# Kernel tuning notes

Hardware: AMD Instinct MI355X
Metric: run time of the kernel (lower is better)

## Reference

```python
import jax, jax.numpy as jnp
import numpy as np

B, N_PER, P_PER = 64, 64, 2016   # graphs, nodes/graph, pairs/graph (C(64,2))
IN_DIM, HID, OUT = 64, 128, 10
EDGE_P = 0.125


def _build_graph_structures():
    """Integer preprocessing replicating build_2sets_from_embeddings's
    combinatorics (pairs, iso_type source, triangle-based 2-set edges)."""
    rng = np.random.default_rng(0)
    n, b = N_PER, B
    A = rng.random((b, n, n)) < EDGE_P
    A = np.triu(A, 1)
    A = A | A.transpose(0, 2, 1)                      # symmetric, no self loops
    gs, us, vs = np.nonzero(A)                        # directed edges, both dirs
    edge_index = np.stack([gs * n + us, gs * n + vs]).astype(np.int64)
    batch = np.repeat(np.arange(b), n).astype(np.int64)
    iu, iv = np.triu_indices(n, 1)                    # local pair (u<v) lists
    pidx = np.full((n, n), -1, np.int64)
    pidx[iu, iv] = np.arange(P_PER)
    pidx[iv, iu] = np.arange(P_PER)                   # symmetric lookup = sorted()
    pair_u = (np.arange(b)[:, None] * n + iu[None, :]).ravel().astype(np.int64)
    pair_v = (np.arange(b)[:, None] * n + iv[None, :]).ravel().astype(np.int64)
    iso_type = A[:, iu, iv].astype(np.float32).ravel()[:, None]  # [B*P_PER,1]
    # 2-set edges: pair (u,v) -> sorted(v,w) and sorted(u,w) for every common
    # neighbor w of u and v (matches _build_2set_edges exactly)
    common = A[:, iu, :] & A[:, iv, :]                # (B, P_PER, n)
    g2, ps, ws = np.nonzero(common)
    u, v = iu[ps], iv[ps]
    d1 = pidx[v, ws]
    d2 = pidx[u, ws]
    src = np.concatenate([g2 * P_PER + ps, g2 * P_PER + ps])
    dst = np.concatenate([g2 * P_PER + d1, g2 * P_PER + d2])
    two_edges = np.stack([src, dst]).astype(np.int64)
    two_batch = np.repeat(np.arange(b), P_PER).astype(np.int64)
    return edge_index, batch, pair_u, pair_v, iso_type, two_edges, two_batch


def setup_inputs() -> dict:
    ei, batch, pu, pv, iso, te, tb = _build_graph_structures()
    key = jax.random.key(0)
    ks = jax.random.split(key, 16)
    w = lambda k, i, o: jax.random.normal(k, (i, o), jnp.float32) / np.float32(np.sqrt(i))
    two_in = 2 * HID + 1
    return {
        "x": jax.random.normal(ks[0], (B * N_PER, IN_DIM), jnp.float32),
        "g1_W1_0": w(ks[1], IN_DIM, HID), "g1_W2_0": w(ks[2], IN_DIM, HID),
        "g1_W1_1": w(ks[3], HID, HID),    "g1_W2_1": w(ks[4], HID, HID),
        "g1_W1_2": w(ks[5], HID, HID),    "g1_W2_2": w(ks[6], HID, HID),
        "k_W1_0": w(ks[7], two_in, HID),  "k_W2_0": w(ks[8], two_in, HID),
        "k_W1_1": w(ks[9], HID, HID),     "k_W2_1": w(ks[10], HID, HID),
        "c_W0": w(ks[11], 2 * HID, HID),  "c_b0": jnp.zeros((HID,), jnp.float32),
        "c_W1": w(ks[12], HID, OUT),      "c_b1": jnp.zeros((OUT,), jnp.float32),
        "iso_type": jnp.asarray(iso),
        "edge_index": jnp.asarray(ei), "batch": jnp.asarray(batch),
        "pair_u": jnp.asarray(pu), "pair_v": jnp.asarray(pv),
        "two_edges": jnp.asarray(te), "two_batch": jnp.asarray(tb),
    }


def _mp_layer(h, ei, W1, W2):
    # relu( h @ W1 + scatter_add_{dst}( h[src] @ W2 ) )  -- OneGNNLayer / KSetLayer
    msg = h[ei[0]] @ W2
    agg = jax.ops.segment_sum(msg, ei[1], num_segments=h.shape[0])
    return jax.nn.relu(h @ W1 + agg)


def reference(x, g1_W1_0, g1_W2_0, g1_W1_1, g1_W2_1, g1_W1_2, g1_W2_2,
              k_W1_0, k_W2_0, k_W1_1, k_W2_1,
              c_W0, c_b0, c_W1, c_b1,
              iso_type, edge_index, batch, pair_u, pair_v, two_edges, two_batch):
    h = _mp_layer(x, edge_index, g1_W1_0, g1_W2_0)
    h = _mp_layer(h, edge_index, g1_W1_1, g1_W2_1)
    h = _mp_layer(h, edge_index, g1_W1_2, g1_W2_2)
    graph_emb_1 = jax.ops.segment_sum(h, batch, num_segments=B)
    # 2-set features: [h_u, h_v, iso_type]  -> [P, 2H+1]
    two_x = jnp.concatenate([h[pair_u], h[pair_v], iso_type], axis=1)
    h2 = _mp_layer(two_x, two_edges, k_W1_0, k_W2_0)
    h2 = _mp_layer(h2, two_edges, k_W1_1, k_W2_1)
    graph_emb_2 = jax.ops.segment_sum(h2, two_batch, num_segments=B)
    combined = jnp.concatenate([graph_emb_1, graph_emb_2], axis=1)
    hc = jax.nn.relu(combined @ c_W0 + c_b0)   # Dropout(p=0.5) inactive in eval
    return hc @ c_W1 + c_b1
```

## Files before the change

kernel.cpp:

```cpp
#include <hip/hip_runtime.h>
#include <hip/hip_bf16.h>


typedef short s16x8 __attribute__((ext_vector_type(8)));
typedef float f32x4 __attribute__((ext_vector_type(4)));

__device__ __forceinline__ unsigned short f2bf(float f) {
  union { float f; unsigned u; } x; x.f = f;
  unsigned r = (x.u + 0x7fffu + ((x.u >> 16) & 1u)) >> 16;
  return (unsigned short)r;
}
__device__ __forceinline__ float bf2f(unsigned short h) {
  union { unsigned u; float f; } x; x.u = ((unsigned)h) << 16;
  return x.f;
}
__device__ __forceinline__ float4 ldbf4(const unsigned short* p) {
  ushort4 q = *(const ushort4*)p;
  return make_float4(bf2f(q.x), bf2f(q.y), bf2f(q.z), bf2f(q.w));
}
__device__ __forceinline__ void stbf4(unsigned short* p, float4 v) {
  ushort4 q;
  q.x = f2bf(v.x); q.y = f2bf(v.y); q.z = f2bf(v.z); q.w = f2bf(v.w);
  *(ushort4*)p = q;
}
__device__ __forceinline__ float4 ld4(const float* p) { return *(const float4*)p; }

template<int KCS, int ASTR>
__device__ __forceinline__ void mfma_dual_lds(
    const unsigned short* A, const unsigned short* Wfrag,
    f32x4 (&accA)[8], f32x4 (&accB)[8])
{
  const int lane = threadIdx.x & 63;
  const int wv = threadIdx.x >> 6;
  const int row = wv * 16 + (lane & 15);
  const int k0 = (lane >> 4) << 3;
  const unsigned short* ap = A + row * ASTR + k0;
  const unsigned short* wp = Wfrag + (size_t)lane * 8;
#pragma unroll
  for (int i = 0; i < 8; ++i) { accA[i] = (f32x4)0.f; accB[i] = (f32x4)0.f; }
#pragma unroll
  for (int kc = 0; kc < KCS; ++kc) {
    s16x8 af = *(const s16x8*)(ap + kc * 32);
#pragma unroll
    for (int nt = 0; nt < 8; ++nt) {
      s16x8 b0 = *(const s16x8*)(wp + ((size_t)((nt)*KCS + kc) << 9));
      s16x8 b1 = *(const s16x8*)(wp + ((size_t)((8 + nt) * KCS + kc) << 9));
      accA[nt] = __builtin_amdgcn_mfma_f32_16x16x32_bf16(af, b0, accA[nt], 0, 0, 0);
      accB[nt] = __builtin_amdgcn_mfma_f32_16x16x32_bf16(af, b1, accB[nt], 0, 0, 0);
    }
  }
}

__device__ __forceinline__ void epi_lds(const f32x4 (&accA)[8], const f32x4 (&accB)[8],
    unsigned short (*preS)[136], unsigned short (*msgS)[136])
{
  const int lane = threadIdx.x & 63;
  const int wv = threadIdx.x >> 6;
  const int col = lane & 15;
  const int r0 = wv * 16 + ((lane >> 4) << 2);
  __syncthreads();
#pragma unroll
  for (int nt = 0; nt < 8; ++nt)
#pragma unroll
    for (int r = 0; r < 4; ++r) {
      preS[r0 + r][nt * 16 + col] = f2bf(accA[nt][r]);
      msgS[r0 + r][nt * 16 + col] = f2bf(accB[nt][r]);
    }
  __syncthreads();
}

__device__ __forceinline__ void epi_global(const f32x4 (&accA)[8], const f32x4 (&accB)[8],
    unsigned short (*sOut)[136], unsigned short* Ca, unsigned short* Cb, long tile)
{
  const int tid = threadIdx.x;
  const int lane = tid & 63;
  const int wv = tid >> 6;
  const int col = lane & 15;
  const int r0 = wv * 16 + ((lane >> 4) << 2);
  const long rowBase = tile * 64;
#pragma unroll
  for (int sel = 0; sel < 2; ++sel) {
    __syncthreads();
#pragma unroll
    for (int nt = 0; nt < 8; ++nt) {
#pragma unroll
      for (int r = 0; r < 4; ++r)
        sOut[r0 + r][nt * 16 + col] = f2bf(sel ? accB[nt][r] : accA[nt][r]);
    }
    __syncthreads();
    unsigned short* C = sel ? Cb : Ca;
#pragma unroll
    for (int i = 0; i < 4; ++i) {
      int fi = tid + i * 256;
      int row = fi >> 4;
      int c8 = fi & 15;
      *(uint4*)(C + (rowBase + row) * 128 + c8 * 8) = *(uint4*)&sOut[row][c8 * 8];
    }
  }
}

struct NArgs {
  const float* x;
  const int* ei;
  const int* gstart;
  const unsigned short *Wf0, *Wf1, *Wf2, *Wf3, *Wf4;
  unsigned short *HU1, *HV1, *HU2, *HV2;
  float* ge1;
  int E1;
};

__global__ __launch_bounds__(256) void node_stage(NArgs a)
{
  __shared__ __align__(16) unsigned short hS[64][136];
  __shared__ __align__(16) unsigned short preS[64][136];
  __shared__ __align__(16) unsigned short msgS[64][136];
  __shared__ int ldeg[64], lcur[64], loff[65];
  __shared__ unsigned short ledge[1024];
  __shared__ float sge[128];

  const int b = blockIdx.x;
  const int t = threadIdx.x;
  const int base = b * 64;

  const int es = a.gstart[b], ee = a.gstart[b + 1];
  if (t < 64) ldeg[t] = 0;
  if (t < 128) sge[t] = 0.f;
  __syncthreads();
  for (int i = es + t; i < ee; i += 256)
    atomicAdd(&ldeg[a.ei[a.E1 + i] - base], 1);
  __syncthreads();
  if (t < 64) {
    int v = ldeg[t], s = v;
#pragma unroll
    for (int d = 1; d < 64; d <<= 1) {
      int o = __shfl_up(s, d, 64);
      if (t >= d) s += o;
    }
    loff[t] = s - v;
    lcur[t] = s - v;
    if (t == 63) loff[64] = s;
  }
  unsigned short* xs = &preS[0][0];
  for (int i = t; i < 64 * 64; i += 256) {
    int r = i >> 6, c = i & 63;
    xs[r * 72 + c] = f2bf(a.x[(size_t)(base + r) * 64 + c]);
  }
  __syncthreads();
  for (int i = es + t; i < ee; i += 256) {
    int s = a.ei[i] - base, d = a.ei[a.E1 + i] - base;
    int pos = atomicAdd(&lcur[d], 1);
    ledge[pos] = (unsigned short)s;
  }
  __syncthreads();

  f32x4 accA[8], accB[8];
  const int grp = t >> 5, f = (t & 31) * 4;

  mfma_dual_lds<2, 72>(xs, a.Wf0, accA, accB);
  epi_lds(accA, accB, preS, msgS);
  for (int r = grp; r < 64; r += 8) {
    float4 acc = ldbf4(&preS[r][f]);
    int j1 = loff[r + 1];
    for (int j = loff[r]; j < j1; ++j) {
      float4 m = ldbf4(&msgS[ledge[j]][f]);
      acc.x += m.x; acc.y += m.y; acc.z += m.z; acc.w += m.w;
    }
    stbf4(&hS[r][f], make_float4(fmaxf(acc.x, 0.f), fmaxf(acc.y, 0.f),
                                 fmaxf(acc.z, 0.f), fmaxf(acc.w, 0.f)));
  }
  __syncthreads();

  mfma_dual_lds<4, 136>(&hS[0][0], a.Wf1, accA, accB);
  epi_lds(accA, accB, preS, msgS);
  for (int r = grp; r < 64; r += 8) {
    float4 acc = ldbf4(&preS[r][f]);
    int j1 = loff[r + 1];
    for (int j = loff[r]; j < j1; ++j) {
      float4 m = ldbf4(&msgS[ledge[j]][f]);
      acc.x += m.x; acc.y += m.y; acc.z += m.z; acc.w += m.w;
    }
    stbf4(&hS[r][f], make_float4(fmaxf(acc.x, 0.f), fmaxf(acc.y, 0.f),
                                 fmaxf(acc.z, 0.f), fmaxf(acc.w, 0.f)));
  }
  __syncthreads();

  mfma_dual_lds<4, 136>(&hS[0][0], a.Wf2, accA, accB);
  epi_lds(accA, accB, preS, msgS);
  {
    float4 g = make_float4(0.f, 0.f, 0.f, 0.f);
    for (int r = grp; r < 64; r += 8) {
      float4 acc = ldbf4(&preS[r][f]);
      int j1 = loff[r + 1];
      for (int j = loff[r]; j < j1; ++j) {
        float4 m = ldbf4(&msgS[ledge[j]][f]);
        acc.x += m.x; acc.y += m.y; acc.z += m.z; acc.w += m.w;
      }
      float4 o = make_float4(fmaxf(acc.x, 0.f), fmaxf(acc.y, 0.f),
                             fmaxf(acc.z, 0.f), fmaxf(acc.w, 0.f));
      stbf4(&hS[r][f], o);
      g.x += o.x; g.y += o.y; g.z += o.z; g.w += o.w;
    }
    atomicAdd(&sge[f + 0], g.x);
    atomicAdd(&sge[f + 1], g.y);
    atomicAdd(&sge[f + 2], g.z);
    atomicAdd(&sge[f + 3], g.w);
  }
  __syncthreads();
  if (t < 128) a.ge1[b * 128 + t] = sge[t];

  mfma_dual_lds<4, 136>(&hS[0][0], a.Wf3, accA, accB);
  epi_global(accA, accB, preS, a.HU1, a.HU2, b);
  mfma_dual_lds<4, 136>(&hS[0][0], a.Wf4, accA, accB);
  epi_global(accA, accB, preS, a.HV1, a.HV2, b);
}

struct PrepArgs {
  const float* wa[6];
  const float* wb[6];
  unsigned short* Wf[6];
  float* ge2;
  const int* te; int E2;
  int* degP;
  const int* ei; int E1;
  int* gstart;
  int nCnt;
};

__global__ void prep(PrepArgs p)
{
  int bb = blockIdx.x, t = threadIdx.x;
  if (bb < 88) {
    int gid = bb * 256 + t;
    if (gid < 22528) {
      int pi, local, kcs, kclog;
      if (gid < 2048) { pi = 0; local = gid; kcs = 2; kclog = 1; }
      else { int r = gid - 2048; pi = 1 + (r >> 12); local = r & 4095; kcs = 4; kclog = 2; }
      int lane = local & 63;
      int t1 = local >> 6;
      int kc = t1 & (kcs - 1);
      int t2 = t1 >> kclog;
      int nt = t2 & 7;
      int wsel = t2 >> 3;
      const float* W = wsel ? p.wb[pi] : p.wa[pi];
      int k0 = kc * 32 + ((lane >> 4) << 3);
      int n = nt * 16 + (lane & 15);
      unsigned short tmp[8];
#pragma unroll
      for (int j = 0; j < 8; ++j) tmp[j] = f2bf(W[(size_t)(k0 + j) * 128 + n]);
      *(uint4*)(p.Wf[pi] + (size_t)local * 8) = *(uint4*)tmp;
    }
  } else if (bb < 120) {
    int i = (bb - 88) * 256 + t;
    if (i < 8192) p.ge2[i] = 0.f;
  } else if (bb < 120 + p.nCnt) {
    int e = (bb - 120) * 256 + t;
    if (e < p.E2) atomicAdd(&p.degP[p.te[p.E2 + e]], 1);
  } else {
    int e = (bb - 120 - p.nCnt) * 256 + t;
    if (e <= p.E1) {
      int ge = (e < p.E1) ? (p.ei[e] >> 6) : 64;
      int gp = (e > 0) ? (p.ei[e - 1] >> 6) : -1;
      for (int g = gp + 1; g <= ge; ++g) p.gstart[g] = e;
    }
  }
}

__global__ __launch_bounds__(256) void scan_reduce(const int* __restrict__ deg,
                                                   int* __restrict__ bsum, int n)
{
  __shared__ int s[256];
  int b = blockIdx.x, t = threadIdx.x;
  int base = b * 1024;
  int v = 0;
#pragma unroll
  for (int i = 0; i < 4; ++i) {
    int idx = base + t + i * 256;
    if (idx < n) v += deg[idx];
  }
  s[t] = v;
  __syncthreads();
  for (int d = 128; d > 0; d >>= 1) {
    if (t < d) s[t] += s[t + d];
    __syncthreads();
  }
  if (t == 0) bsum[b] = s[0];
}

__global__ __launch_bounds__(1024) void scan_partials(int* __restrict__ bsum, int nb)
{
  __shared__ int s[1024];
  int t = threadIdx.x;
  s[t] = (t < nb) ? bsum[t] : 0;
  __syncthreads();
  for (int d = 1; d < 1024; d <<= 1) {
    int v = (t >= d) ? s[t - d] : 0;
    __syncthreads();
    s[t] += v;
    __syncthreads();
  }
  if (t < nb) bsum[t] = (t == 0) ? 0 : s[t - 1];
  if (t == 1023) bsum[nb] = s[1023];
}

__global__ __launch_bounds__(256) void scan_final(const int* __restrict__ deg,
                                                  const int* __restrict__ bsum,
                                                  int* __restrict__ off,
                                                  int* __restrict__ cur, int n, int nb)
{
  __shared__ int s[256];
  int b = blockIdx.x, t = threadIdx.x;
  int base = b * 1024 + t * 4;
  int v0 = 0, v1 = 0, v2 = 0, v3 = 0;
  if (base + 0 < n) v0 = deg[base + 0];
  if (base + 1 < n) v1 = deg[base + 1];
  if (base + 2 < n) v2 = deg[base + 2];
  if (base + 3 < n) v3 = deg[base + 3];
  s[t] = v0 + v1 + v2 + v3;
  __syncthreads();
  for (int d = 1; d < 256; d <<= 1) {
    int v = (t >= d) ? s[t - d] : 0;
    __syncthreads();
    s[t] += v;
    __syncthreads();
  }
  int run = bsum[b] + ((t == 0) ? 0 : s[t - 1]);
  if (base + 0 < n) { off[base + 0] = run; cur[base + 0] = run; run += v0; }
  if (base + 1 < n) { off[base + 1] = run; cur[base + 1] = run; run += v1; }
  if (base + 2 < n) { off[base + 2] = run; cur[base + 2] = run; run += v2; }
  if (base + 3 < n) { off[base + 3] = run; cur[base + 3] = run; run += v3; }
  if (b == 0 && t == 0) off[n] = bsum[nb];
}

__global__ void csr_fill_pair(const int* __restrict__ te, int E2,
                              const int* __restrict__ pu, const int* __restrict__ pv,
                              const float* __restrict__ iso,
                              int* __restrict__ curP, int4* __restrict__ recP)
{
  int e = blockIdx.x * 256 + threadIdx.x;
  if (e >= E2) return;
  int s = te[e], d = te[E2 + e];
  int pos = atomicAdd(&curP[d], 1);
  recP[pos] = make_int4(pu[s], pv[s], __float_as_int(iso[s]), s);
}

struct TGArgs {
  const unsigned short *HU1, *HV1, *HU2, *HV2;
  const float *iso, *w1iso, *w2iso;
  const int *pu, *pv, *off;
  const int4* rec;
  const unsigned short* Wf5;
  unsigned short *PRE2, *MSG2;
};

__global__ __launch_bounds__(256) void two0_gemm(TGArgs a)
{
  __shared__ __align__(16) unsigned short hS[64][136];
  __shared__ int sOff[65];
  __shared__ int sPu[64], sPv[64];
  __shared__ float sIso[64];
  const int t = threadIdx.x;
  const long tile = blockIdx.x;
  const int grp = t >> 5, f = (t & 31) * 4;
  const int pbase = (int)(tile * 64);

  if (t < 65) sOff[t] = a.off[pbase + t];
  if (t >= 64 && t < 128)  sPu[t - 64]  = a.pu[pbase + t - 64];
  if (t >= 128 && t < 192) sPv[t - 128] = a.pv[pbase + t - 128];
  if (t >= 192)            sIso[t - 192] = a.iso[pbase + t - 192];
  __syncthreads();

  float4 wi1 = ld4(a.w1iso + f);
  float4 wi2 = ld4(a.w2iso + f);

#pragma unroll
  for (int pass = 0; pass < 4; ++pass) {
    int rA = grp * 8 + pass * 2;
    int rB = rA + 1;
    float isA = sIso[rA], isB = sIso[rB];
    float4 a1 = ldbf4(a.HU1 + (size_t)sPu[rA] * 128 + f);
    float4 b1 = ldbf4(a.HV1 + (size_t)sPv[rA] * 128 + f);
    float4 a2 = ldbf4(a.HU1 + (size_t)sPu[rB] * 128 + f);
    float4 b2 = ldbf4(a.HV1 + (size_t)sPv[rB] * 128 + f);
    float4 accA, accB;
    accA.x = a1.x + b1.x + isA * wi1.x;
    accA.y = a1.y + b1.y + isA * wi1.y;
    accA.z = a1.z + b1.z + isA * wi1.z;
    accA.w = a1.w + b1.w + isA * wi1.w;
    accB.x = a2.x + b2.x + isB * wi1.x;
    accB.y = a2.y + b2.y + isB * wi1.y;
    accB.z = a2.z + b2.z + isB * wi1.z;
    accB.w = a2.w + b2.w + isB * wi1.w;
    int jA = sOff[rA], eA = sOff[rA + 1];
    int jB = sOff[rB], eB = sOff[rB + 1];
    while (jA < eA && jB < eB) {
      int4 qA = a.rec[jA++];
      int4 qB = a.rec[jB++];
      float4 muA = ldbf4(a.HU2 + (size_t)qA.x * 128 + f);
      float4 mvA = ldbf4(a.HV2 + (size_t)qA.y * 128 + f);
      float4 muB = ldbf4(a.HU2 + (size_t)qB.x * 128 + f);
      float4 mvB = ldbf4(a.HV2 + (size_t)qB.y * 128 + f);
      float iA = __int_as_float(qA.z), iB = __int_as_float(qB.z);
      accA.x += muA.x + mvA.x + iA * wi2.x;
      accA.y += muA.y + mvA.y + iA * wi2.y;
      accA.z += muA.z + mvA.z + iA * wi2.z;
      accA.w += muA.w + mvA.w + iA * wi2.w;
      accB.x += muB.x + mvB.x + iB * wi2.x;
      accB.y += muB.y + mvB.y + iB * wi2.y;
      accB.z += muB.z + mvB.z + iB * wi2.z;
      accB.w += muB.w + mvB.w + iB * wi2.w;
    }
    for (; jA + 1 < eA; jA += 2) {
      int4 q0 = a.rec[jA], q1 = a.rec[jA + 1];
      float4 mu0 = ldbf4(a.HU2 + (size_t)q0.x * 128 + f);
      float4 mv0 = ldbf4(a.HV2 + (size_t)q0.y * 128 + f);
      float4 mu1 = ldbf4(a.HU2 + (size_t)q1.x * 128 + f);
      float4 mv1 = ldbf4(a.HV2 + (size_t)q1.y * 128 + f);
      float i0 = __int_as_float(q0.z), i1 = __int_as_float(q1.z);
      accA.x += mu0.x + mv0.x + i0 * wi2.x + mu1.x + mv1.x + i1 * wi2.x;
      accA.y += mu0.y + mv0.y + i0 * wi2.y + mu1.y + mv1.y + i1 * wi2.y;
      accA.z += mu0.z + mv0.z + i0 * wi2.z + mu1.z + mv1.z + i1 * wi2.z;
      accA.w += mu0.w + mv0.w + i0 * wi2.w + mu1.w + mv1.w + i1 * wi2.w;
    }
    if (jA < eA) {
      int4 q0 = a.rec[jA];
      float4 mu0 = ldbf4(a.HU2 + (size_t)q0.x * 128 + f);
      float4 mv0 = ldbf4(a.HV2 + (size_t)q0.y * 128 + f);
      float i0 = __int_as_float(q0.z);
      accA.x += mu0.x + mv0.x + i0 * wi2.x;
      accA.y += mu0.y + mv0.y + i0 * wi2.y;
      accA.z += mu0.z + mv0.z + i0 * wi2.z;
      accA.w += mu0.w + mv0.w + i0 * wi2.w;
    }
    for (; jB + 1 < eB; jB += 2) {
      int4 q0 = a.rec[jB], q1 = a.rec[jB + 1];
      float4 mu0 = ldbf4(a.HU2 + (size_t)q0.x * 128 + f);
      float4 mv0 = ldbf4(a.HV2 + (size_t)q0.y * 128 + f);
      float4 mu1 = ldbf4(a.HU2 + (size_t)q1.x * 128 + f);
      float4 mv1 = ldbf4(a.HV2 + (size_t)q1.y * 128 + f);
      float i0 = __int_as_float(q0.z), i1 = __int_as_float(q1.z);
      accB.x += mu0.x + mv0.x + i0 * wi2.x + mu1.x + mv1.x + i1 * wi2.x;
      accB.y += mu0.y + mv0.y + i0 * wi2.y + mu1.y + mv1.y + i1 * wi2.y;
      accB.z += mu0.z + mv0.z + i0 * wi2.z + mu1.z + mv1.z + i1 * wi2.z;
      accB.w += mu0.w + mv0.w + i0 * wi2.w + mu1.w + mv1.w + i1 * wi2.w;
    }
    if (jB < eB) {
      int4 q0 = a.rec[jB];
      float4 mu0 = ldbf4(a.HU2 + (size_t)q0.x * 128 + f);
      float4 mv0 = ldbf4(a.HV2 + (size_t)q0.y * 128 + f);
      float i0 = __int_as_float(q0.z);
      accB.x += mu0.x + mv0.x + i0 * wi2.x;
      accB.y += mu0.y + mv0.y + i0 * wi2.y;
      accB.z += mu0.z + mv0.z + i0 * wi2.z;
      accB.w += mu0.w + mv0.w + i0 * wi2.w;
    }
    stbf4(&hS[rA][f], make_float4(fmaxf(accA.x, 0.f), fmaxf(accA.y, 0.f),
                                  fmaxf(accA.z, 0.f), fmaxf(accA.w, 0.f)));
    stbf4(&hS[rB][f], make_float4(fmaxf(accB.x, 0.f), fmaxf(accB.y, 0.f),
                                  fmaxf(accB.z, 0.f), fmaxf(accB.w, 0.f)));
  }
  __syncthreads();

  f32x4 accA[8], accB[8];
  mfma_dual_lds<4, 136>(&hS[0][0], a.Wf5, accA, accB);
  epi_global(accA, accB, hS, a.PRE2, a.MSG2, tile);
}

__global__ __launch_bounds__(256) void gather_segsum(
    const unsigned short* __restrict__ pre, const unsigned short* __restrict__ msg,
    const int* __restrict__ off, const int4* __restrict__ rec,
    float* __restrict__ ge2, int ppg)
{
  __shared__ float sF[128];
  __shared__ int sOff[127];
  int t = threadIdx.x;
  int c = blockIdx.x & 7;
  int k = blockIdx.x >> 3;
  int g = c + 8 * (k & 7);
  int sub = k >> 3;
  int r0 = g * ppg + sub * 126;
  if (t < 128) sF[t] = 0.f;
  if (t < 127) sOff[t] = off[r0 + t];
  __syncthreads();
  int grp = t >> 5, f = (t & 31) * 4;
  const int lim = 126;
  int rbeg = grp * 16;
  int rend = rbeg + 16; if (rend > lim) rend = lim;
  float4 gacc = make_float4(0.f, 0.f, 0.f, 0.f);
  for (int rr = rbeg; rr < rend; rr += 2) {
    int rA = rr, rB = rr + 1;
    bool vB = (rB < rend);
    float4 accA = ldbf4(pre + (size_t)(r0 + rA) * 128 + f);
    float4 accB = vB ? ldbf4(pre + (size_t)(r0 + rB) * 128 + f)
                     : make_float4(0.f, 0.f, 0.f, 0.f);
    int jA = sOff[rA], eA = sOff[rA + 1];
    int jB = vB ? sOff[rB] : 0, eB = vB ? sOff[rB + 1] : 0;
    while (jA < eA && jB < eB) {
      int sA = rec[jA++].w;
      int sB = rec[jB++].w;
      float4 mA = ldbf4(msg + (size_t)sA * 128 + f);
      float4 mB = ldbf4(msg + (size_t)sB * 128 + f);
      accA.x += mA.x; accA.y += mA.y; accA.z += mA.z; accA.w += mA.w;
      accB.x += mB.x; accB.y += mB.y; accB.z += mB.z; accB.w += mB.w;
    }
    for (; jA + 1 < eA; jA += 2) {
      int s0 = rec[jA].w, s1 = rec[jA + 1].w;
      float4 m0 = ldbf4(msg + (size_t)s0 * 128 + f);
      float4 m1 = ldbf4(msg + (size_t)s1 * 128 + f);
      accA.x += m0.x + m1.x; accA.y += m0.y + m1.y;
      accA.z += m0.z + m1.z; accA.w += m0.w + m1.w;
    }
    if (jA < eA) {
      float4 m0 = ldbf4(msg + (size_t)rec[jA].w * 128 + f);
      accA.x += m0.x; accA.y += m0.y; accA.z += m0.z; accA.w += m0.w;
    }
    for (; jB + 1 < eB; jB += 2) {
      int s0 = rec[jB].w, s1 = rec[jB + 1].w;
      float4 m0 = ldbf4(msg + (size_t)s0 * 128 + f);
      float4 m1 = ldbf4(msg + (size_t)s1 * 128 + f);
      accB.x += m0.x + m1.x; accB.y += m0.y + m1.y;
      accB.z += m0.z + m1.z; accB.w += m0.w + m1.w;
    }
    if (jB < eB) {
      float4 m0 = ldbf4(msg + (size_t)rec[jB].w * 128 + f);
      accB.x += m0.x; accB.y += m0.y; accB.z += m0.z; accB.w += m0.w;
    }
    gacc.x += fmaxf(accA.x, 0.f); gacc.y += fmaxf(accA.y, 0.f);
    gacc.z += fmaxf(accA.z, 0.f); gacc.w += fmaxf(accA.w, 0.f);
    if (vB) {
      gacc.x += fmaxf(accB.x, 0.f); gacc.y += fmaxf(accB.y, 0.f);
      gacc.z += fmaxf(accB.z, 0.f); gacc.w += fmaxf(accB.w, 0.f);
    }
  }
  atomicAdd(&sF[f + 0], gacc.x);
  atomicAdd(&sF[f + 1], gacc.y);
  atomicAdd(&sF[f + 2], gacc.z);
  atomicAdd(&sF[f + 3], gacc.w);
  __syncthreads();
  if (t < 128) atomicAdd(&ge2[g * 128 + t], sF[t]);
}

__global__ void classifier(const float* __restrict__ ge1, const float* __restrict__ ge2,
                           const float* __restrict__ W0, const float* __restrict__ b0,
                           const float* __restrict__ W1, const float* __restrict__ b1,
                           float* __restrict__ out)
{
  __shared__ float comb[256];
  __shared__ float hc[128];
  int g = blockIdx.x, t = threadIdx.x;
  comb[t]       = ge1[g * 128 + t];
  comb[t + 128] = ge2[g * 128 + t];
  __syncthreads();
  float s = b0[t];
  for (int k = 0; k < 256; ++k) s += comb[k] * W0[k * 128 + t];
  hc[t] = fmaxf(s, 0.f);
  __syncthreads();
  if (t < 10) {
    float s2 = b1[t];
    for (int k = 0; k < 128; ++k) s2 += hc[k] * W1[k * 10 + t];
    out[g * 10 + t] = s2;
  }
}

extern "C" void kernel_launch(void* const* d_in, const int* in_sizes, int n_in,
                              void* d_out, int out_size, void* d_ws, size_t ws_size,
                              hipStream_t stream)
{
  (void)n_in; (void)out_size; (void)ws_size;
  const float* x       = (const float*)d_in[0];
  const float* g1_W1_0 = (const float*)d_in[1];
  const float* g1_W2_0 = (const float*)d_in[2];
  const float* g1_W1_1 = (const float*)d_in[3];
  const float* g1_W2_1 = (const float*)d_in[4];
  const float* g1_W1_2 = (const float*)d_in[5];
  const float* g1_W2_2 = (const float*)d_in[6];
  const float* k_W1_0  = (const float*)d_in[7];
  const float* k_W2_0  = (const float*)d_in[8];
  const float* k_W1_1  = (const float*)d_in[9];
  const float* k_W2_1  = (const float*)d_in[10];
  const float* c_W0    = (const float*)d_in[11];
  const float* c_b0    = (const float*)d_in[12];
  const float* c_W1    = (const float*)d_in[13];
  const float* c_b1    = (const float*)d_in[14];
  const float* iso     = (const float*)d_in[15];
  const int*   ei      = (const int*)d_in[16];
  const int*   pu      = (const int*)d_in[18];
  const int*   pv      = (const int*)d_in[19];
  const int*   te      = (const int*)d_in[20];

  const int N  = in_sizes[0] / 64;
  const int E1 = in_sizes[16] / 2;
  const int P  = in_sizes[18];
  const int E2 = in_sizes[20] / 2;
  const int B  = 64;
  const int ppg = P / B;

  const size_t NH = (size_t)N * 128;
  const size_t PH = (size_t)P * 128;

  float* ge1 = (float*)d_ws;
  float* ge2 = ge1 + 8192;
  unsigned short* HU1 = (unsigned short*)(ge2 + 8192);
  unsigned short* HV1 = HU1 + NH;
  unsigned short* HU2 = HV1 + NH;
  unsigned short* HV2 = HU2 + NH;
  unsigned short* PRE2 = HV2 + NH;
  unsigned short* MSG2 = PRE2 + PH;
  unsigned short* Wf0  = MSG2 + PH;
  unsigned short* Wf1  = Wf0 + 16384;
  unsigned short* Wf2  = Wf1 + 32768;
  unsigned short* Wf3  = Wf2 + 32768;
  unsigned short* Wf4  = Wf3 + 32768;
  unsigned short* Wf5  = Wf4 + 32768;

  size_t ipOff = ((size_t)((char*)(Wf5 + 32768) - (char*)d_ws) + 15) & ~(size_t)15;
  int4* recP   = (int4*)((char*)d_ws + ipOff);
  int* degP    = (int*)(recP + E2);
  int* offP    = degP + P;
  int* curP    = offP + P + 1;
  int* bsumP   = curP + P;
  int* gstartN = bsumP + 128;

  const int nbP  = (P + 1023) / 1024;
  const int nCnt = (E2 + 255) / 256;
  const int nBnd = (E1 + 256) / 256;

  hipMemsetAsync(degP, 0, (size_t)P * 4, stream);

  PrepArgs pa;
  pa.wa[0] = g1_W1_0;           pa.wb[0] = g1_W2_0;
  pa.wa[1] = g1_W1_1;           pa.wb[1] = g1_W2_1;
  pa.wa[2] = g1_W1_2;           pa.wb[2] = g1_W2_2;
  pa.wa[3] = k_W1_0;            pa.wb[3] = k_W2_0;
  pa.wa[4] = k_W1_0 + 128*128;  pa.wb[4] = k_W2_0 + 128*128;
  pa.wa[5] = k_W1_1;            pa.wb[5] = k_W2_1;
  pa.Wf[0] = Wf0; pa.Wf[1] = Wf1; pa.Wf[2] = Wf2;
  pa.Wf[3] = Wf3; pa.Wf[4] = Wf4; pa.Wf[5] = Wf5;
  pa.ge2 = ge2; pa.te = te; pa.E2 = E2; pa.degP = degP;
  pa.ei = ei; pa.E1 = E1; pa.gstart = gstartN; pa.nCnt = nCnt;
  prep<<<120 + nCnt + nBnd, 256, 0, stream>>>(pa);

  scan_reduce<<<nbP, 256, 0, stream>>>(degP, bsumP, P);
  scan_partials<<<1, 1024, 0, stream>>>(bsumP, nbP);
  scan_final<<<nbP, 256, 0, stream>>>(degP, bsumP, offP, curP, P, nbP);
  csr_fill_pair<<<nCnt, 256, 0, stream>>>(te, E2, pu, pv, iso, curP, recP);

  NArgs na;
  na.x = x; na.ei = ei; na.gstart = gstartN; na.E1 = E1;
  na.Wf0 = Wf0; na.Wf1 = Wf1; na.Wf2 = Wf2; na.Wf3 = Wf3; na.Wf4 = Wf4;
  na.HU1 = HU1; na.HU2 = HU2; na.HV1 = HV1; na.HV2 = HV2;
  na.ge1 = ge1;
  node_stage<<<B, 256, 0, stream>>>(na);

  TGArgs ta;
  ta.HU1 = HU1; ta.HV1 = HV1; ta.HU2 = HU2; ta.HV2 = HV2;
  ta.iso = iso; ta.w1iso = k_W1_0 + 256 * 128; ta.w2iso = k_W2_0 + 256 * 128;
  ta.pu = pu; ta.pv = pv; ta.off = offP; ta.rec = recP;
  ta.Wf5 = Wf5; ta.PRE2 = PRE2; ta.MSG2 = MSG2;
  two0_gemm<<<P / 64, 256, 0, stream>>>(ta);

  gather_segsum<<<B * 16, 256, 0, stream>>>(PRE2, MSG2, offP, recP, ge2, ppg);

  classifier<<<B, 128, 0, stream>>>(ge1, ge2, c_W0, c_b0, c_W1, c_b1, (float*)d_out);
}
```

Baseline: 326.5 us.

## Tile two0_gemm per graph and stage node features and CSR records in LDS

Blocks of two0_gemm now each cover 63 pairs from a single graph, so that graph's 64 HU2/HV2 rows can be copied into shared memory once and the per-edge gathers read from LDS instead of global memory. The block's CSR edge records are also staged into LDS, with a global fallback past a fixed cap. Block ids are swizzled so neighbouring blocks land on different graphs. The epilogue is rewritten inline to handle partial tiles, which pads with zero rows and leaves some MFMA work unused; the larger LDS footprint may lower occupancy.

Result: no change. 327.4 us (+0.3%).

```diff
diff --git a/kernel.cpp b/kernel.cpp
--- a/kernel.cpp
+++ b/kernel.cpp
@@ -343,6 +343,8 @@
   recP[pos] = make_int4(pu[s], pv[s], __float_as_int(iso[s]), s);
 }
 
+#define RECAP 1024
+
 struct TGArgs {
   const unsigned short *HU1, *HV1, *HU2, *HV2;
   const float *iso, *w1iso, *w2iso;
@@ -350,23 +352,46 @@
   const int4* rec;
   const unsigned short* Wf5;
   unsigned short *PRE2, *MSG2;
+  int ppg;
 };
 
 __global__ __launch_bounds__(256) void two0_gemm(TGArgs a)
 {
   __shared__ __align__(16) unsigned short hS[64][136];
-  __shared__ int sOff[65];
-  __shared__ int sPu[64], sPv[64];
-  __shared__ float sIso[64];
+  __shared__ __align__(16) unsigned short sHU2[64][136];
+  __shared__ __align__(16) unsigned short sHV2[64][136];
+  __shared__ __align__(16) int4 sRec[RECAP];
+  __shared__ int sOff[64];
+  __shared__ int sPu[63], sPv[63];
+  __shared__ float sIso[63];
+
   const int t = threadIdx.x;
-  const long tile = blockIdx.x;
+  const int bid = blockIdx.x;
+  const int g = (bid & 7) + 8 * ((bid >> 3) & 7);
+  const int sub = bid >> 6;
+  const int p0 = g * a.ppg + sub * 63;
+  const int rows = (a.ppg - sub * 63 < 63) ? (a.ppg - sub * 63) : 63;
   const int grp = t >> 5, f = (t & 31) * 4;
-  const int pbase = (int)(tile * 64);
-
-  if (t < 65) sOff[t] = a.off[pbase + t];
-  if (t >= 64 && t < 128)  sPu[t - 64]  = a.pu[pbase + t - 64];
-  if (t >= 128 && t < 192) sPv[t - 128] = a.pv[pbase + t - 128];
-  if (t >= 192)            sIso[t - 192] = a.iso[pbase + t - 192];
+
+  if (t < rows) sPu[t] = a.pu[p0 + t];
+  else if (t >= 64 && t - 64 < rows) sPv[t - 64] = a.pv[p0 + t - 64];
+  else if (t >= 128 && t - 128 < rows) sIso[t - 128] = a.iso[p0 + t - 128];
+  else if (t >= 192 && t - 192 <= rows) sOff[t - 192] = a.off[p0 + t - 192];
+  {
+    const unsigned short* gHU2 = a.HU2 + (size_t)g * 64 * 128;
+    const unsigned short* gHV2 = a.HV2 + (size_t)g * 64 * 128;
+#pragma unroll
+    for (int i = t; i < 1024; i += 256) {
+      int r = i >> 4, c8 = i & 15;
+      *(uint4*)&sHU2[r][c8 * 8] = *(const uint4*)(gHU2 + r * 128 + c8 * 8);
+      *(uint4*)&sHV2[r][c8 * 8] = *(const uint4*)(gHV2 + r * 128 + c8 * 8);
+    }
+  }
+  __syncthreads();
+  const int eBase = sOff[0];
+  const int eCnt = sOff[rows] - eBase;
+  for (int i = t; i < eCnt && i < RECAP; i += 256)
+    sRec[i] = a.rec[eBase + i];
   __syncthreads();
 
   float4 wi1 = ld4(a.w1iso + f);
@@ -374,31 +399,37 @@
 
 #pragma unroll
   for (int pass = 0; pass < 4; ++pass) {
-    int rA = grp * 8 + pass * 2;
-    int rB = rA + 1;
-    float isA = sIso[rA], isB = sIso[rB];
-    float4 a1 = ldbf4(a.HU1 + (size_t)sPu[rA] * 128 + f);
-    float4 b1 = ldbf4(a.HV1 + (size_t)sPv[rA] * 128 + f);
-    float4 a2 = ldbf4(a.HU1 + (size_t)sPu[rB] * 128 + f);
-    float4 b2 = ldbf4(a.HV1 + (size_t)sPv[rB] * 128 + f);
-    float4 accA, accB;
-    accA.x = a1.x + b1.x + isA * wi1.x;
-    accA.y = a1.y + b1.y + isA * wi1.y;
-    accA.z = a1.z + b1.z + isA * wi1.z;
-    accA.w = a1.w + b1.w + isA * wi1.w;
-    accB.x = a2.x + b2.x + isB * wi1.x;
-    accB.y = a2.y + b2.y + isB * wi1.y;
-    accB.z = a2.z + b2.z + isB * wi1.z;
-    accB.w = a2.w + b2.w + isB * wi1.w;
-    int jA = sOff[rA], eA = sOff[rA + 1];
-    int jB = sOff[rB], eB = sOff[rB + 1];
+    int rA = grp + pass * 16;
+    int rB = rA + 8;
+    bool vA = rA < rows, vB = rB < rows;
+    float4 accA = make_float4(0.f, 0.f, 0.f, 0.f), accB = accA;
+    if (vA) {
+      float is0 = sIso[rA];
+      float4 a1 = ldbf4(a.HU1 + (size_t)sPu[rA] * 128 + f);
+      float4 b1 = ldbf4(a.HV1 + (size_t)sPv[rA] * 128 + f);
+      accA.x = a1.x + b1.x + is0 * wi1.x;
+      accA.y = a1.y + b1.y + is0 * wi1.y;
+      accA.z = a1.z + b1.z + is0 * wi1.z;
+      accA.w = a1.w + b1.w + is0 * wi1.w;
+    }
+    if (vB) {
+      float is0 = sIso[rB];
+      float4 a1 = ldbf4(a.HU1 + (size_t)sPu[rB] * 128 + f);
+      float4 b1 = ldbf4(a.HV1 + (size_t)sPv[rB] * 128 + f);
+      accB.x = a1.x + b1.x + is0 * wi1.x;
+      accB.y = a1.y + b1.y + is0 * wi1.y;
+      accB.z = a1.z + b1.z + is0 * wi1.z;
+      accB.w = a1.w + b1.w + is0 * wi1.w;
+    }
+    int jA = vA ? sOff[rA] - eBase : 0, eA = vA ? sOff[rA + 1] - eBase : 0;
+    int jB = vB ? sOff[rB] - eBase : 0, eB = vB ? sOff[rB + 1] - eBase : 0;
     while (jA < eA && jB < eB) {
-      int4 qA = a.rec[jA++];
-      int4 qB = a.rec[jB++];
-      float4 muA = ldbf4(a.HU2 + (size_t)qA.x * 128 + f);
-      float4 mvA = ldbf4(a.HV2 + (size_t)qA.y * 128 + f);
-      float4 muB = ldbf4(a.HU2 + (size_t)qB.x * 128 + f);
-      float4 mvB = ldbf4(a.HV2 + (size_t)qB.y * 128 + f);
+      int4 qA = (jA < RECAP) ? sRec[jA] : a.rec[eBase + jA]; ++jA;
+      int4 qB = (jB < RECAP) ? sRec[jB] : a.rec[eBase + jB]; ++jB;
+      float4 muA = ldbf4(&sHU2[qA.x & 63][f]);
+      float4 mvA = ldbf4(&sHV2[qA.y & 63][f]);
+      float4 muB = ldbf4(&sHU2[qB.x & 63][f]);
+      float4 mvB = ldbf4(&sHV2[qB.y & 63][f]);
       float iA = __int_as_float(qA.z), iB = __int_as_float(qB.z);
       accA.x += muA.x + mvA.x + iA * wi2.x;
       accA.y += muA.y + mvA.y + iA * wi2.y;
@@ -409,60 +440,64 @@
       accB.z += muB.z + mvB.z + iB * wi2.z;
       accB.w += muB.w + mvB.w + iB * wi2.w;
     }
-    for (; jA + 1 < eA; jA += 2) {
-      int4 q0 = a.rec[jA], q1 = a.rec[jA + 1];
-      float4 mu0 = ldbf4(a.HU2 + (size_t)q0.x * 128 + f);
-      float4 mv0 = ldbf4(a.HV2 + (size_t)q0.y * 128 + f);
-      float4 mu1 = ldbf4(a.HU2 + (size_t)q1.x * 128 + f);
-      float4 mv1 = ldbf4(a.HV2 + (size_t)q1.y * 128 + f);
-      float i0 = __int_as_float(q0.z), i1 = __int_as_float(q1.z);
-      accA.x += mu0.x + mv0.x + i0 * wi2.x + mu1.x + mv1.x + i1 * wi2.x;
-      accA.y += mu0.y + mv0.y + i0 * wi2.y + mu1.y + mv1.y + i1 * wi2.y;
-      accA.z += mu0.z + mv0.z + i0 * wi2.z + mu1.z + mv1.z + i1 * wi2.z;
-      accA.w += mu0.w + mv0.w + i0 * wi2.w + mu1.w + mv1.w + i1 * wi2.w;
-    }
-    if (jA < eA) {
-      int4 q0 = a.rec[jA];
-      float4 mu0 = ldbf4(a.HU2 + (size_t)q0.x * 128 + f);
-      float4 mv0 = ldbf4(a.HV2 + (size_t)q0.y * 128 + f);
+    for (; jA < eA; ++jA) {
+      int4 q0 = (jA < RECAP) ? sRec[jA] : a.rec[eBase + jA];
+      float4 mu0 = ldbf4(&sHU2[q0.x & 63][f]);
+      float4 mv0 = ldbf4(&sHV2[q0.y & 63][f]);
       float i0 = __int_as_float(q0.z);
       accA.x += mu0.x + mv0.x + i0 * wi2.x;
       accA.y += mu0.y + mv0.y + i0 * wi2.y;
       accA.z += mu0.z + mv0.z + i0 * wi2.z;
       accA.w += mu0.w + mv0.w + i0 * wi2.w;
     }
-    for (; jB + 1 < eB; jB += 2) {
-      int4 q0 = a.rec[jB], q1 = a.rec[jB + 1];
-      float4 mu0 = ldbf4(a.HU2 + (size_t)q0.x * 128 + f);
-      float4 mv0 = ldbf4(a.HV2 + (size_t)q0.y * 128 + f);
-      float4 mu1 = ldbf4(a.HU2 + (size_t)q1.x * 128 + f);
-      float4 mv1 = ldbf4(a.HV2 + (size_t)q1.y * 128 + f);
-      float i0 = __int_as_float(q0.z), i1 = __int_as_float(q1.z);
-      accB.x += mu0.x + mv0.x + i0 * wi2.x + mu1.x + mv1.x + i1 * wi2.x;
-      accB.y += mu0.y + mv0.y + i0 * wi2.y + mu1.y + mv1.y + i1 * wi2.y;
-      accB.z += mu0.z + mv0.z + i0 * wi2.z + mu1.z + mv1.z + i1 * wi2.z;
-      accB.w += mu0.w + mv0.w + i0 * wi2.w + mu1.w + mv1.w + i1 * wi2.w;
-    }
-    if (jB < eB) {
-      int4 q0 = a.rec[jB];
-      float4 mu0 = ldbf4(a.HU2 + (size_t)q0.x * 128 + f);
-      float4 mv0 = ldbf4(a.HV2 + (size_t)q0.y * 128 + f);
+    for (; jB < eB; ++jB) {
+      int4 q0 = (jB < RECAP) ? sRec[jB] : a.rec[eBase + jB];
+      float4 mu0 = ldbf4(&sHU2[q0.x & 63][f]);
+      float4 mv0 = ldbf4(&sHV2[q0.y & 63][f]);
       float i0 = __int_as_float(q0.z);
       accB.x += mu0.x + mv0.x + i0 * wi2.x;
       accB.y += mu0.y + mv0.y + i0 * wi2.y;
       accB.z += mu0.z + mv0.z + i0 * wi2.z;
       accB.w += mu0.w + mv0.w + i0 * wi2.w;
     }
-    stbf4(&hS[rA][f], make_float4(fmaxf(accA.x, 0.f), fmaxf(accA.y, 0.f),
-                                  fmaxf(accA.z, 0.f), fmaxf(accA.w, 0.f)));
-    stbf4(&hS[rB][f], make_float4(fmaxf(accB.x, 0.f), fmaxf(accB.y, 0.f),
-                                  fmaxf(accB.z, 0.f), fmaxf(accB.w, 0.f)));
-  }
+    if (vA) stbf4(&hS[rA][f], make_float4(fmaxf(accA.x, 0.f), fmaxf(accA.y, 0.f),
+                                          fmaxf(accA.z, 0.f), fmaxf(accA.w, 0.f)));
+    if (vB) stbf4(&hS[rB][f], make_float4(fmaxf(accB.x, 0.f), fmaxf(accB.y, 0.f),
+                                          fmaxf(accB.z, 0.f), fmaxf(accB.w, 0.f)));
+  }
+  for (int r = rows + grp; r < 64; r += 8)
+    stbf4(&hS[r][f], make_float4(0.f, 0.f, 0.f, 0.f));
   __syncthreads();
 
   f32x4 accA[8], accB[8];
   mfma_dual_lds<4, 136>(&hS[0][0], a.Wf5, accA, accB);
-  epi_global(accA, accB, hS, a.PRE2, a.MSG2, tile);
+
+  {
+    const int lane = t & 63;
+    const int wv = t >> 6;
+    const int col = lane & 15;
+    const int r0 = wv * 16 + ((lane >> 4) << 2);
+#pragma unroll
+    for (int sel = 0; sel < 2; ++sel) {
+      __syncthreads();
+#pragma unroll
+      for (int nt = 0; nt < 8; ++nt) {
+#pragma unroll
+        for (int r = 0; r < 4; ++r)
+          hS[r0 + r][nt * 16 + col] = f2bf(sel ? accB[nt][r] : accA[nt][r]);
+      }
+      __syncthreads();
+      unsigned short* C = sel ? a.MSG2 : a.PRE2;
+#pragma unroll
+      for (int i = 0; i < 4; ++i) {
+        int fi = t + i * 256;
+        int row = fi >> 4;
+        int c8 = fi & 15;
+        if (row < rows)
+          *(uint4*)(C + (size_t)(p0 + row) * 128 + c8 * 8) = *(uint4*)&hS[row][c8 * 8];
+      }
+    }
+  }
 }
 
 __global__ __launch_bounds__(256) void gather_segsum(
@@ -623,6 +658,7 @@
   const int nbP  = (P + 1023) / 1024;
   const int nCnt = (E2 + 255) / 256;
   const int nBnd = (E1 + 256) / 256;
+  const int subsPG = (ppg + 62) / 63;
 
   hipMemsetAsync(degP, 0, (size_t)P * 4, stream);
 
@@ -655,8 +691,8 @@
   ta.HU1 = HU1; ta.HV1 = HV1; ta.HU2 = HU2; ta.HV2 = HV2;
   ta.iso = iso; ta.w1iso = k_W1_0 + 256 * 128; ta.w2iso = k_W2_0 + 256 * 128;
   ta.pu = pu; ta.pv = pv; ta.off = offP; ta.rec = recP;
-  ta.Wf5 = Wf5; ta.PRE2 = PRE2; ta.MSG2 = MSG2;
-  two0_gemm<<<P / 64, 256, 0, stream>>>(ta);
+  ta.Wf5 = Wf5; ta.PRE2 = PRE2; ta.MSG2 = MSG2; ta.ppg = ppg;
+  two0_gemm<<<B * subsPG, 256, 0, stream>>>(ta);
 
   gather_segsum<<<B * 16, 256, 0, stream>>>(PRE2, MSG2, offP, recP, ge2, ppg);
 
```
